# Kernel tuning notes

Hardware: AMD Instinct MI355X
Metric: run time of the kernel (lower is better)

The kernel has to match this reference:

```python
import jax, jax.numpy as jnp
import numpy as np

ALIGN_CORNERS = False  # matches init_kwargs


def setup_inputs() -> dict:
    key = jax.random.key(0)
    k1, k2 = jax.random.split(key)
    features = jax.random.normal(k1, (8, 128, 128, 256), dtype=jnp.float32)
    grid = jax.random.uniform(k2, (8, 16384, 2), dtype=jnp.float32)  # values in [0, 1)
    return {"features": features, "grid": grid}


def reference(features, grid):
    # features: [B, H, W, C] (NHWC), grid: [B, P, 2] with values in [0, 1], last axis (x, y)
    B, H, W, C = features.shape
    # pad H and W by 1 on each side so out-of-range corner taps read zeros
    safe = jnp.pad(features, ((0, 0), (1, 1), (1, 1), (0, 0))).astype(grid.dtype)

    g = grid[..., ::-1]  # reverse last axis -> (y, x) matching (H, W)
    size = jnp.asarray([H, W], dtype=grid.dtype)
    if ALIGN_CORNERS:
        g = g * (size - 1)
    else:
        g = (2.0 * g * size - 1.0) / 2.0

    bounds = jnp.asarray([H + 1, W + 1], dtype=jnp.int32)  # per-axis clip max in padded map
    batch_idx = jnp.arange(B)[:, None]  # [B, 1], broadcasts over P

    def lookup(coords):
        c = jnp.clip(coords.astype(jnp.int32) + 1, 0, bounds)  # shift into padded coords
        return safe[batch_idx, c[..., 0], c[..., 1]]  # [B, P, C]

    g_nw = jnp.floor(g)
    g_ne = g_nw + jnp.asarray([1.0, 0.0], g.dtype)
    g_sw = g_nw + jnp.asarray([0.0, 1.0], g.dtype)
    g_se = g_nw + jnp.asarray([1.0, 1.0], g.dtype)

    one = jnp.asarray([1.0, -1.0], g.dtype)
    w_nw = jnp.prod(g_se - g, axis=-1, keepdims=True)
    w_ne = jnp.prod((g_sw - g) * one, axis=-1, keepdims=True)
    w_sw = jnp.prod((g_ne - g) * -one, axis=-1, keepdims=True)
    w_se = jnp.prod(g - g_nw, axis=-1, keepdims=True)

    result = (lookup(g_nw) * w_nw + lookup(g_ne) * w_ne
              + lookup(g_sw) * w_sw + lookup(g_se) * w_se)
    return result.astype(features.dtype)  # [B, P, C]
```

## Files before the change

### kernel.cpp

```cpp
#include <hip/hip_runtime.h>


constexpr int B = 8, H = 128, W = 128, C = 256, P = 16384;
constexpr int PPW = 4;
constexpr int TS = 32;
constexpr int TPS = W / TS;
constexpr int TPB = TPS * TPS;
constexpr int NPTS = B * P;
constexpr int NBLK = NPTS / (4 * PPW);

typedef float f32x4 __attribute__((ext_vector_type(4)));

__device__ __forceinline__ int tile16(float gx, float gy) {
    int ix = (int)floorf(gx * (float)W - 0.5f);
    int iy = (int)floorf(gy * (float)H - 0.5f);
    ix = min(max(ix, 0), W - 1);
    iy = min(max(iy, 0), H - 1);
    return (iy / TS) * TPS + (ix / TS);
}

__global__ __launch_bounds__(1024) void bucket_sort_kernel(
    const float* __restrict__ grid, int* __restrict__ perm)
{
    __shared__ int h[TPB];
    __shared__ int pre[TPB];
    const int tid  = threadIdx.x;
    const int base = blockIdx.x * P;
    if (tid < TPB) h[tid] = 0;
    __syncthreads();

    int myTile[16], myRank[16];
    const float2* g2 = reinterpret_cast<const float2*>(grid);
    #pragma unroll
    for (int i = 0; i < 16; ++i) {
        const int pt = base + i * 1024 + tid;
        const float2 g = g2[pt];
        const int t = tile16(g.x, g.y);
        myTile[i] = t;
        myRank[i] = atomicAdd(&h[t], 1);
    }
    __syncthreads();
    if (tid == 0) {
        int acc = 0;
        #pragma unroll
        for (int t = 0; t < TPB; ++t) { pre[t] = acc; acc += h[t]; }
    }
    __syncthreads();
    #pragma unroll
    for (int i = 0; i < 16; ++i)
        perm[base + pre[myTile[i]] + myRank[i]] = base + i * 1024 + tid;
}

__global__ __launch_bounds__(256) void point_sample_kernel(
    const float* __restrict__ features,
    const float* __restrict__ grid,
    const int* __restrict__ perm,
    float* __restrict__ out)
{
    const int wave = threadIdx.x >> 6;
    const int lane = threadIdx.x & 63;
    int bid = blockIdx.x;
    bid = (bid & 7) * (NBLK >> 3) + (bid >> 3);
    const int w = bid * 4 + wave;

    const int4 pv = *reinterpret_cast<const int4*>(perm + w * PPW);
    const int ptv[PPW] = {pv.x, pv.y, pv.z, pv.w};
    const int c = lane * 4;

    int   off[PPW][4];
    float wgt[PPW][4];
    #pragma unroll
    for (int k = 0; k < PPW; ++k) {
        const int pt = ptv[k];
        const int b = pt >> 14;
        const float2 g = reinterpret_cast<const float2*>(grid)[pt];
        const float x = g.x * (float)W - 0.5f;
        const float y = g.y * (float)H - 0.5f;
        const float fx = floorf(x), fy = floorf(y);
        const int ix = (int)fx, iy = (int)fy;
        const float frx = x - fx, fry = y - fy;

        const int x0 = min(max(ix, 0), W - 1);
        const int x1 = min(max(ix + 1, 0), W - 1);
        const int y0 = min(max(iy, 0), H - 1);
        const int y1 = min(max(iy + 1, 0), H - 1);
        const float mx0 = (ix >= 0 && ix < W)         ? 1.f : 0.f;
        const float mx1 = (ix + 1 >= 0 && ix + 1 < W) ? 1.f : 0.f;
        const float my0 = (iy >= 0 && iy < H)         ? 1.f : 0.f;
        const float my1 = (iy + 1 >= 0 && iy + 1 < H) ? 1.f : 0.f;

        wgt[k][0] = (1.f - fry) * (1.f - frx) * my0 * mx0;
        wgt[k][1] = (1.f - fry) * frx         * my0 * mx1;
        wgt[k][2] = fry         * (1.f - frx) * my1 * mx0;
        wgt[k][3] = fry         * frx         * my1 * mx1;
        const int fbase = b * (H * W * C) + c;
        off[k][0] = fbase + (y0 * W + x0) * C;
        off[k][1] = fbase + (y0 * W + x1) * C;
        off[k][2] = fbase + (y1 * W + x0) * C;
        off[k][3] = fbase + (y1 * W + x1) * C;
    }

    float4 v[PPW][4];
    #pragma unroll
    for (int k = 0; k < PPW; ++k)
        #pragma unroll
        for (int j = 0; j < 4; ++j)
            v[k][j] = *reinterpret_cast<const float4*>(features + off[k][j]);

    #pragma unroll
    for (int k = 0; k < PPW; ++k) {
        f32x4 acc = (f32x4)0.f;
        #pragma unroll
        for (int j = 0; j < 4; ++j) {
            const float wq = wgt[k][j];
            acc.x += wq * v[k][j].x;
            acc.y += wq * v[k][j].y;
            acc.z += wq * v[k][j].z;
            acc.w += wq * v[k][j].w;
        }
        f32x4* op = reinterpret_cast<f32x4*>(out + (size_t)ptv[k] * C + c);
        __builtin_nontemporal_store(acc, op);
    }
}

__global__ __launch_bounds__(256) void point_sample_direct(
    const float* __restrict__ features,
    const float* __restrict__ grid,
    float* __restrict__ out)
{
    const int wave = threadIdx.x >> 6;
    const int lane = threadIdx.x & 63;
    const int pt = blockIdx.x * 4 + wave;
    const int b = pt >> 14;
    const float2 g = reinterpret_cast<const float2*>(grid)[pt];
    const float x = g.x * (float)W - 0.5f;
    const float y = g.y * (float)H - 0.5f;
    const float fx = floorf(x), fy = floorf(y);
    const int ix = (int)fx, iy = (int)fy;
    const float frx = x - fx, fry = y - fy;
    const float* fb = features + (size_t)b * H * W * C;
    const int c = lane * 4;
    f32x4 acc = (f32x4)0.f;
    #pragma unroll
    for (int dy = 0; dy < 2; ++dy) {
        const int hy = iy + dy;
        const bool vy = (hy >= 0) && (hy < H);
        #pragma unroll
        for (int dx = 0; dx < 2; ++dx) {
            const int wx = ix + dx;
            if (vy && (wx >= 0) && (wx < W)) {
                const float wgt = dy ? (dx ? fry * frx : fry * (1.f - frx))
                                     : (dx ? (1.f - fry) * frx : (1.f - fry) * (1.f - frx));
                const float4 vv = *reinterpret_cast<const float4*>(
                    fb + ((size_t)hy * W + wx) * C + c);
                acc.x += wgt * vv.x; acc.y += wgt * vv.y;
                acc.z += wgt * vv.z; acc.w += wgt * vv.w;
            }
        }
    }
    f32x4* op = reinterpret_cast<f32x4*>(out + (size_t)pt * C + c);
    __builtin_nontemporal_store(acc, op);
}

extern "C" void kernel_launch(void* const* d_in, const int* in_sizes, int n_in,
                              void* d_out, int out_size, void* d_ws, size_t ws_size,
                              hipStream_t stream) {
    const float* features = (const float*)d_in[0];
    const float* grid     = (const float*)d_in[1];
    float* out            = (float*)d_out;

    const size_t need = (size_t)NPTS * sizeof(int);
    if (ws_size < need) {
        point_sample_direct<<<NPTS / 4, 256, 0, stream>>>(features, grid, out);
        return;
    }

    int* perm = (int*)d_ws;

    bucket_sort_kernel <<<B, 1024, 0, stream>>>(grid, perm);
    point_sample_kernel<<<NBLK, 256, 0, stream>>>(features, grid, perm, out);
}
```

Baseline: 55.21 us.

## Split bucket sort into parallel histogram and scatter over segments

The single-block-per-batch bucket sort is replaced by a two-pass counting sort: a histogram kernel over 64 segments, then a scatter kernel that computes global offsets from the per-segment histograms. The scatter also writes grid coordinates in sorted order, so the sampling kernel reads them contiguously with vector loads instead of gathering them. This spreads the sort across more blocks and removes the serial single-thread prefix scan, at the cost of an extra kernel launch and extra workspace traffic.

Measured after the change: 53.21 us. -3.6%, faster.

```diff
diff --git a/kernel.cpp b/kernel.cpp
--- a/kernel.cpp
+++ b/kernel.cpp
@@ -8,6 +8,9 @@
 constexpr int TPB = TPS * TPS;
 constexpr int NPTS = B * P;
 constexpr int NBLK = NPTS / (4 * PPW);
+constexpr int SPB  = 8;
+constexpr int NSEG = B * SPB;
+constexpr int SEGP = P / SPB;
 
 typedef float f32x4 __attribute__((ext_vector_type(4)));
 
@@ -19,41 +22,71 @@
     return (iy / TS) * TPS + (ix / TS);
 }
 
-__global__ __launch_bounds__(1024) void bucket_sort_kernel(
-    const float* __restrict__ grid, int* __restrict__ perm)
+__global__ __launch_bounds__(1024) void histo_kernel(
+    const float* __restrict__ grid, int* __restrict__ hglob)
 {
     __shared__ int h[TPB];
-    __shared__ int pre[TPB];
-    const int tid  = threadIdx.x;
-    const int base = blockIdx.x * P;
+    const int tid = threadIdx.x;
+    const int seg = blockIdx.x;
+    const int base = seg * SEGP;
     if (tid < TPB) h[tid] = 0;
     __syncthreads();
-
-    int myTile[16], myRank[16];
     const float2* g2 = reinterpret_cast<const float2*>(grid);
     #pragma unroll
-    for (int i = 0; i < 16; ++i) {
-        const int pt = base + i * 1024 + tid;
+    for (int i = 0; i < 2; ++i) {
+        const float2 g = g2[base + i * 1024 + tid];
+        atomicAdd(&h[tile16(g.x, g.y)], 1);
+    }
+    __syncthreads();
+    if (tid < TPB) hglob[seg * TPB + tid] = h[tid];
+}
+
+__global__ __launch_bounds__(1024) void scatter_kernel(
+    const float* __restrict__ grid, const int* __restrict__ hglob,
+    int* __restrict__ perm, float2* __restrict__ gsorted)
+{
+    __shared__ int h[TPB];
+    __shared__ int base[TPB];
+    const int tid = threadIdx.x;
+    const int seg = blockIdx.x;
+    const int b   = seg / SPB;
+    const int sib = seg - b * SPB;
+    const int pbase = seg * SEGP;
+
+    if (tid < TPB) {
+        h[tid] = 0;
+        const int* hb = hglob + b * SPB * TPB;
+        int tot_before = 0;
+        for (int t = 0; t < TPB; ++t) {
+            if (t < tid) {
+                int s = 0;
+                #pragma unroll
+                for (int q = 0; q < SPB; ++q) s += hb[q * TPB + t];
+                tot_before += s;
+            }
+        }
+        int intra = 0;
+        for (int q = 0; q < sib; ++q) intra += hb[q * TPB + tid];
+        base[tid] = b * P + tot_before + intra;
+    }
+    __syncthreads();
+
+    const float2* g2 = reinterpret_cast<const float2*>(grid);
+    #pragma unroll
+    for (int i = 0; i < 2; ++i) {
+        const int pt = pbase + i * 1024 + tid;
         const float2 g = g2[pt];
         const int t = tile16(g.x, g.y);
-        myTile[i] = t;
-        myRank[i] = atomicAdd(&h[t], 1);
-    }
-    __syncthreads();
-    if (tid == 0) {
-        int acc = 0;
-        #pragma unroll
-        for (int t = 0; t < TPB; ++t) { pre[t] = acc; acc += h[t]; }
-    }
-    __syncthreads();
-    #pragma unroll
-    for (int i = 0; i < 16; ++i)
-        perm[base + pre[myTile[i]] + myRank[i]] = base + i * 1024 + tid;
+        const int r = atomicAdd(&h[t], 1);
+        const int pos = base[t] + r;
+        perm[pos] = pt;
+        gsorted[pos] = g;
+    }
 }
 
 __global__ __launch_bounds__(256) void point_sample_kernel(
     const float* __restrict__ features,
-    const float* __restrict__ grid,
+    const float* __restrict__ gs,
     const int* __restrict__ perm,
     float* __restrict__ out)
 {
@@ -65,17 +98,20 @@
 
     const int4 pv = *reinterpret_cast<const int4*>(perm + w * PPW);
     const int ptv[PPW] = {pv.x, pv.y, pv.z, pv.w};
+    const float* gf = gs + (size_t)w * 2 * PPW;
+    const float4 gA = *reinterpret_cast<const float4*>(gf);
+    const float4 gB = *reinterpret_cast<const float4*>(gf + 4);
+    const float gxv[PPW] = {gA.x, gA.z, gB.x, gB.z};
+    const float gyv[PPW] = {gA.y, gA.w, gB.y, gB.w};
     const int c = lane * 4;
 
     int   off[PPW][4];
     float wgt[PPW][4];
     #pragma unroll
     for (int k = 0; k < PPW; ++k) {
-        const int pt = ptv[k];
-        const int b = pt >> 14;
-        const float2 g = reinterpret_cast<const float2*>(grid)[pt];
-        const float x = g.x * (float)W - 0.5f;
-        const float y = g.y * (float)H - 0.5f;
+        const int b = ptv[k] >> 14;
+        const float x = gxv[k] * (float)W - 0.5f;
+        const float y = gyv[k] * (float)H - 0.5f;
         const float fx = floorf(x), fy = floorf(y);
         const int ix = (int)fx, iy = (int)fy;
         const float frx = x - fx, fry = y - fy;
@@ -169,14 +205,20 @@
     const float* grid     = (const float*)d_in[1];
     float* out            = (float*)d_out;
 
-    const size_t need = (size_t)NPTS * sizeof(int);
+    const size_t need = (size_t)NPTS * sizeof(int) +
+                        (size_t)NPTS * sizeof(float2) +
+                        (size_t)NSEG * TPB * sizeof(int);
     if (ws_size < need) {
         point_sample_direct<<<NPTS / 4, 256, 0, stream>>>(features, grid, out);
         return;
     }
 
-    int* perm = (int*)d_ws;
-
-    bucket_sort_kernel <<<B, 1024, 0, stream>>>(grid, perm);
-    point_sample_kernel<<<NBLK, 256, 0, stream>>>(features, grid, perm, out);
-}
+    int*    perm    = (int*)d_ws;
+    float2* gsorted = (float2*)(perm + NPTS);
+    int*    hglob   = (int*)(gsorted + NPTS);
+
+    histo_kernel  <<<NSEG, 1024, 0, stream>>>(grid, hglob);
+    scatter_kernel<<<NSEG, 1024, 0, stream>>>(grid, hglob, perm, gsorted);
+    point_sample_kernel<<<NBLK, 256, 0, stream>>>(
+        features, reinterpret_cast<const float*>(gsorted), perm, out);
+}
```

## Split bucket sort into per-segment blocks and emit sorted grid coordinates

Applied to the files above, without the earlier changes.

The bucket sort now runs as 64 blocks (8 segments per batch) instead of one block per batch. Each block rebuilds the full per-batch tile histogram plus a histogram of the preceding segments, then scatters only its own 2048 points. The sort also writes the grid coordinates in sorted order, so the sampling kernel reads them contiguously instead of gathering them through perm. The cost is redundant histogram work in every block and an extra workspace buffer for the sorted coordinates; the fallback direct kernel also switches to a normal store.

Result: faster. 52.31 us (-5.2%).

```diff
diff --git a/kernel.cpp b/kernel.cpp
--- a/kernel.cpp
+++ b/kernel.cpp
@@ -8,6 +8,9 @@
 constexpr int TPB = TPS * TPS;
 constexpr int NPTS = B * P;
 constexpr int NBLK = NPTS / (4 * PPW);
+constexpr int SPB  = 8;
+constexpr int NSEG = B * SPB;
+constexpr int SEGP = P / SPB;
 
 typedef float f32x4 __attribute__((ext_vector_type(4)));
 
@@ -19,41 +22,57 @@
     return (iy / TS) * TPS + (ix / TS);
 }
 
-__global__ __launch_bounds__(1024) void bucket_sort_kernel(
-    const float* __restrict__ grid, int* __restrict__ perm)
+__global__ __launch_bounds__(1024) void sort_kernel(
+    const float* __restrict__ grid, int* __restrict__ perm,
+    float2* __restrict__ gsorted)
 {
-    __shared__ int h[TPB];
-    __shared__ int pre[TPB];
+    __shared__ int h_total[TPB], h_intra[TPB], h_rank[TPB], base[TPB];
     const int tid  = threadIdx.x;
-    const int base = blockIdx.x * P;
-    if (tid < TPB) h[tid] = 0;
+    const int seg  = blockIdx.x;
+    const int b    = seg >> 3;
+    const int sib  = seg & 7;
+    const int bbase = b * P;
+    const int pbase = seg * SEGP;
+
+    if (tid < TPB) { h_total[tid] = 0; h_intra[tid] = 0; h_rank[tid] = 0; }
     __syncthreads();
 
-    int myTile[16], myRank[16];
     const float2* g2 = reinterpret_cast<const float2*>(grid);
+    float2 myG[2]; int myT[2];
     #pragma unroll
     for (int i = 0; i < 16; ++i) {
-        const int pt = base + i * 1024 + tid;
+        const int pt = bbase + i * 1024 + tid;
         const float2 g = g2[pt];
         const int t = tile16(g.x, g.y);
-        myTile[i] = t;
-        myRank[i] = atomicAdd(&h[t], 1);
+        atomicAdd(&h_total[t], 1);
+        if (i < sib * 2) atomicAdd(&h_intra[t], 1);
+        if (i == sib * 2)     { myG[0] = g; myT[0] = t; }
+        if (i == sib * 2 + 1) { myG[1] = g; myT[1] = t; }
     }
     __syncthreads();
+
     if (tid == 0) {
         int acc = 0;
         #pragma unroll
-        for (int t = 0; t < TPB; ++t) { pre[t] = acc; acc += h[t]; }
+        for (int t = 0; t < TPB; ++t) {
+            base[t] = bbase + acc + h_intra[t];
+            acc += h_total[t];
+        }
     }
     __syncthreads();
-    #pragma unroll
-    for (int i = 0; i < 16; ++i)
-        perm[base + pre[myTile[i]] + myRank[i]] = base + i * 1024 + tid;
+
+    #pragma unroll
+    for (int j = 0; j < 2; ++j) {
+        const int r = atomicAdd(&h_rank[myT[j]], 1);
+        const int pos = base[myT[j]] + r;
+        perm[pos] = pbase + j * 1024 + tid;
+        gsorted[pos] = myG[j];
+    }
 }
 
 __global__ __launch_bounds__(256) void point_sample_kernel(
     const float* __restrict__ features,
-    const float* __restrict__ grid,
+    const float* __restrict__ gs,
     const int* __restrict__ perm,
     float* __restrict__ out)
 {
@@ -65,17 +84,20 @@
 
     const int4 pv = *reinterpret_cast<const int4*>(perm + w * PPW);
     const int ptv[PPW] = {pv.x, pv.y, pv.z, pv.w};
+    const float* gf = gs + (size_t)w * 2 * PPW;
+    const float4 gA = *reinterpret_cast<const float4*>(gf);
+    const float4 gB = *reinterpret_cast<const float4*>(gf + 4);
+    const float gxv[PPW] = {gA.x, gA.z, gB.x, gB.z};
+    const float gyv[PPW] = {gA.y, gA.w, gB.y, gB.w};
     const int c = lane * 4;
 
     int   off[PPW][4];
     float wgt[PPW][4];
     #pragma unroll
     for (int k = 0; k < PPW; ++k) {
-        const int pt = ptv[k];
-        const int b = pt >> 14;
-        const float2 g = reinterpret_cast<const float2*>(grid)[pt];
-        const float x = g.x * (float)W - 0.5f;
-        const float y = g.y * (float)H - 0.5f;
+        const int b = ptv[k] >> 14;
+        const float x = gxv[k] * (float)W - 0.5f;
+        const float y = gyv[k] * (float)H - 0.5f;
         const float fx = floorf(x), fy = floorf(y);
         const int ix = (int)fx, iy = (int)fy;
         const float frx = x - fx, fry = y - fy;
@@ -159,7 +181,7 @@
         }
     }
     f32x4* op = reinterpret_cast<f32x4*>(out + (size_t)pt * C + c);
-    __builtin_nontemporal_store(acc, op);
+    *op = acc;
 }
 
 extern "C" void kernel_launch(void* const* d_in, const int* in_sizes, int n_in,
@@ -169,14 +191,17 @@
     const float* grid     = (const float*)d_in[1];
     float* out            = (float*)d_out;
 
-    const size_t need = (size_t)NPTS * sizeof(int);
+    const size_t need = (size_t)NPTS * sizeof(int) +
+                        (size_t)NPTS * sizeof(float2);
     if (ws_size < need) {
         point_sample_direct<<<NPTS / 4, 256, 0, stream>>>(features, grid, out);
         return;
     }
 
-    int* perm = (int*)d_ws;
-
-    bucket_sort_kernel <<<B, 1024, 0, stream>>>(grid, perm);
-    point_sample_kernel<<<NBLK, 256, 0, stream>>>(features, grid, perm, out);
-}
+    int*    perm    = (int*)d_ws;
+    float2* gsorted = (float2*)(perm + NPTS);
+
+    sort_kernel<<<NSEG, 1024, 0, stream>>>(grid, perm, gsorted);
+    point_sample_kernel<<<NBLK, 256, 0, stream>>>(
+        features, reinterpret_cast<const float*>(gsorted), perm, out);
+}
```
